# Optimization experiments

Hardware: AMD Instinct MI355X
Metric: run time of the kernel (lower is better)

## Reference

```python
import jax, jax.numpy as jnp
import numpy as np

B, NS, D, H, L, NQ, NK = 32, 4096, 256, 4, 6, 512, 1024
DH = D // H
SCALE = 1.0 / np.sqrt(DH)


def _ln(x, scale, bias, eps=1e-5):
    m = jnp.mean(x, axis=-1, keepdims=True)
    v = jnp.mean((x - m) ** 2, axis=-1, keepdims=True)
    return (x - m) * jax.lax.rsqrt(v + eps) * scale + bias


def setup_inputs() -> dict:
    key = jax.random.key(0)
    ks = jax.random.split(key, 12)
    d = {
        'update_tensor': jax.random.normal(ks[0], (B, NS, D), jnp.float32) * 0.1,
        'emb_table': jax.random.normal(ks[1], (NS + 1, D), jnp.float32) * 0.1,
        'mask_logits': jax.random.uniform(ks[2], (L, NQ, NK), jnp.float32),
        'Wq': jax.random.normal(ks[3], (D, D), jnp.float32) * 0.05,
        'Wk': jax.random.normal(ks[4], (D, D), jnp.float32) * 0.05,
        'Wv': jax.random.normal(ks[5], (D, D), jnp.float32) * 0.05,
        'Wo': jax.random.normal(ks[6], (D, D), jnp.float32) * 0.05,
        'W1': jax.random.normal(ks[7], (D, D), jnp.float32) * 0.05,
        'b1': jnp.zeros((D,), jnp.float32),
        'W2': jax.random.normal(ks[8], (D, D), jnp.float32) * 0.05,
        'b2': jnp.zeros((D,), jnp.float32),
        'sys_scale': jnp.ones((D,), jnp.float32),
        'sys_bias': jnp.zeros((D,), jnp.float32),
        'eff_scale': jnp.ones((D,), jnp.float32),
        'eff_bias': jnp.zeros((D,), jnp.float32),
        'inner_scale': jnp.ones((D,), jnp.float32),
        'inner_bias': jnp.zeros((D,), jnp.float32),
        'outer_scale': jnp.ones((D,), jnp.float32),
        'outer_bias': jnp.zeros((D,), jnp.float32),
        'query_idx': jax.random.randint(ks[9], (L, NQ), 0, NS).astype(jnp.int32),
        'key_idx': jax.random.randint(ks[10], (L, NK), 0, NS).astype(jnp.int32),
    }
    return d


def _hitr(q, k, mask, Wq, Wk, Wv, Wo, W1, b1, W2, b2, in_s, in_b, out_s, out_b):
    # q: [B,NQ,D] (pre-normed), k: [B,NK,D], mask: [NQ,NK] bool
    Q = jnp.einsum('bqd,de->bqe', q, Wq).reshape(B, NQ, H, DH)
    K = jnp.einsum('bkd,de->bke', k, Wk).reshape(B, NK, H, DH)
    V = jnp.einsum('bkd,de->bke', k, Wv).reshape(B, NK, H, DH)
    scores = jnp.einsum('bqhd,bkhd->bhqk', Q, K) * SCALE
    scores = jnp.where(mask[None, None], scores, jnp.float32(-1e9))
    attn = jax.nn.softmax(scores, axis=-1)
    ctx = jnp.einsum('bhqk,bkhd->bqhd', attn, V).reshape(B, NQ, D)
    h = _ln(jnp.einsum('bqd,de->bqe', ctx, Wo), in_s, in_b)
    ffn = jnp.einsum('bqd,de->bqe', jax.nn.gelu(jnp.einsum('bqd,de->bqe', h, W1) + b1), W2) + b2
    return _ln(h + ffn, out_s, out_b)


def reference(update_tensor, emb_table, mask_logits, Wq, Wk, Wv, Wo, W1, b1, W2, b2,
              sys_scale, sys_bias, eff_scale, eff_bias, inner_scale, inner_bias,
              outer_scale, outer_bias, query_idx, key_idx):
    update_result = jnp.zeros_like(update_tensor)
    for l in range(L):  # static hierarchy levels
        qi, ki = query_idx[l], key_idx[l]
        mask = mask_logits[l] > 0.5
        q = _ln(emb_table[qi][None] + update_tensor[:, qi], sys_scale, sys_bias)
        k = _ln(emb_table[ki][None] + update_tensor[:, ki], sys_scale, sys_bias)
        res = _ln(_hitr(q, k, mask, Wq, Wk, Wv, Wo, W1, b1, W2, b2,
                        inner_scale, inner_bias, outer_scale, outer_bias),
                  eff_scale, eff_bias)
        update_tensor = update_tensor.at[:, qi].add(res)
        update_result = update_result.at[:, qi].add(res)
    return update_result
```

## Files before the change

kernel.cpp:

```cpp
#include <hip/hip_runtime.h>
#include <cstdint>
#include <cstddef>

#define B_ 32
#define NS_ 4096
#define D_ 256
#define H_ 4
#define L_ 6
#define NQ_ 512
#define NK_ 1024
#define DH_ 64
#define SCALE_ 0.125f

typedef unsigned short ushort_t;
typedef unsigned long long u64_t;
typedef __bf16 bf16x8 __attribute__((ext_vector_type(8)));
typedef float f32x4 __attribute__((ext_vector_type(4)));

__device__ __forceinline__ ushort_t f2bf(float f) {
  unsigned u = __float_as_uint(f);
  u += 0x7fffu + ((u >> 16) & 1u);
  return (ushort_t)(u >> 16);
}

__device__ __forceinline__ void gld16(const void* g, void* l) {
  __builtin_amdgcn_global_load_lds(
      (__attribute__((address_space(1))) void*)(uintptr_t)g,
      (__attribute__((address_space(3))) void*)(uintptr_t)l, 16, 0, 0);
}

__global__ __launch_bounds__(256) void prep_w(
    const float* __restrict__ w0, const float* __restrict__ w1,
    const float* __restrict__ w2, const float* __restrict__ w3,
    const float* __restrict__ w4, const float* __restrict__ w5,
    ushort_t* __restrict__ wt) {
  const int sel = blockIdx.x >> 8;
  const int n = blockIdx.x & 255;
  const int k = threadIdx.x;
  const float* W = sel == 0 ? w0 : sel == 1 ? w1 : sel == 2 ? w2
                 : sel == 3 ? w3 : sel == 4 ? w4 : w5;
  wt[sel * 65536 + n * 256 + k] = f2bf(W[k * 256 + n]);
}

__global__ __launch_bounds__(256) void prep_mask(
    const float* __restrict__ ml, u64_t* __restrict__ mb) {
  const long gid = (long)blockIdx.x * 256 + threadIdx.x;
  const bool m = ml[gid] > 0.5f;
  const u64_t bal = __ballot(m);
  if ((threadIdx.x & 63) == 0) mb[gid >> 6] = bal;
}

__global__ __launch_bounds__(256) void prep_mask2(
    const u64_t* __restrict__ mb, u64_t* __restrict__ pm) {
  const long gid = (long)blockIdx.x * 256 + threadIdx.x;
  const long rowbase = (gid >> 4) << 4;
  const int l16 = (int)(gid & 15);
  u64_t v = 0;
#pragma unroll
  for (int kt = 0; kt < 16; ++kt) {
    const u64_t wsrc = mb[rowbase + kt];
#pragma unroll
    for (int ni = 0; ni < 4; ++ni)
      v |= ((wsrc >> (ni * 16 + l16)) & 1ull) << (kt * 4 + ni);
  }
  pm[gid] = v;
}

__global__ __launch_bounds__(256) void gather_ln(
    const float* __restrict__ ut, const float* __restrict__ emb,
    const int* __restrict__ qidx, const int* __restrict__ kidx,
    const float* __restrict__ sc, const float* __restrict__ bi,
    ushort_t* __restrict__ qn, ushort_t* __restrict__ kn) {
  const int w = threadIdx.x >> 6, lane = threadIdx.x & 63;
  const int R = blockIdx.x * 4 + w;
  int bb, idx;
  ushort_t* dst;
  long drow;
  if (R < B_ * NQ_) {
    bb = R >> 9; idx = qidx[R & (NQ_ - 1)]; dst = qn; drow = R;
  } else {
    const int r2 = R - B_ * NQ_;
    bb = r2 >> 10; idx = kidx[r2 & (NK_ - 1)]; dst = kn; drow = r2;
  }
  const int c0 = lane * 4;
  const float4 e = *(const float4*)(emb + (long)idx * 256 + c0);
  const float4 u = *(const float4*)(ut + ((long)bb * NS_ + idx) * 256 + c0);
  float x0 = e.x + u.x, x1 = e.y + u.y, x2 = e.z + u.z, x3 = e.w + u.w;
  float s1 = x0 + x1 + x2 + x3;
  float s2 = x0 * x0 + x1 * x1 + x2 * x2 + x3 * x3;
#pragma unroll
  for (int off = 1; off < 64; off <<= 1) {
    s1 += __shfl_xor(s1, off);
    s2 += __shfl_xor(s2, off);
  }
  const float mean = s1 * (1.f / 256.f);
  const float inv = rsqrtf(s2 * (1.f / 256.f) - mean * mean + 1e-5f);
  const float4 scv = *(const float4*)(sc + c0);
  const float4 biv = *(const float4*)(bi + c0);
  ushort4 o;
  o.x = f2bf((x0 - mean) * inv * scv.x + biv.x);
  o.y = f2bf((x1 - mean) * inv * scv.y + biv.y);
  o.z = f2bf((x2 - mean) * inv * scv.z + biv.z);
  o.w = f2bf((x3 - mean) * inv * scv.w + biv.w);
  *(ushort4*)(dst + drow * 256 + c0) = o;
}

template <int EPI>
__device__ __forceinline__ void gemm_body(
    const ushort_t* __restrict__ A, const ushort_t* __restrict__ Bt,
    void* __restrict__ Cout, long m0, int n0, ushort_t* lAB) {
  ushort_t* lA = lAB;
  ushort_t* lB = lAB + 8192;
  const int tid = threadIdx.x;
  const int lane = tid & 63, w = tid >> 6;
  const int quad = lane >> 4, l16 = lane & 15;
  const int wm = w & 1, wn = w >> 1;

  f32x4 acc[4][4] = {};

  for (int kt = 0; kt < 4; ++kt) {
    const int k0 = kt * 64;
#pragma unroll
    for (int p = 0; p < 4; ++p) {
      const int ob = p * 4096 + tid * 16;
      const int row = ob >> 7;
      const int chunk = ((ob >> 4) & 7) ^ (row & 7);
      gld16(A + (m0 + row) * 256 + k0 + chunk * 8, (char*)lA + p * 4096 + w * 1024);
      gld16(Bt + (long)(n0 + row) * 256 + k0 + chunk * 8, (char*)lB + p * 4096 + w * 1024);
    }
    __syncthreads();
#pragma unroll
    for (int ki = 0; ki < 2; ++ki) {
      bf16x8 af[4], bfr[4];
#pragma unroll
      for (int i = 0; i < 4; ++i) {
        const int ra = wm * 64 + i * 16 + l16;
        const int ca = (ki * 4 + quad) ^ (ra & 7);
        af[i] = *(const bf16x8*)&lA[ra * 64 + ca * 8];
        const int rb = wn * 64 + i * 16 + l16;
        const int cb = (ki * 4 + quad) ^ (rb & 7);
        bfr[i] = *(const bf16x8*)&lB[rb * 64 + cb * 8];
      }
#pragma unroll
      for (int mi = 0; mi < 4; ++mi)
#pragma unroll
        for (int ni = 0; ni < 4; ++ni)
          acc[mi][ni] = __builtin_amdgcn_mfma_f32_16x16x32_bf16(af[mi], bfr[ni], acc[mi][ni], 0, 0, 0);
    }
    __syncthreads();
  }

  if (EPI == 4) {
    const long b = m0 >> 10;
    const int kvseg = (int)(m0 & 1023);
#pragma unroll
    for (int hg = 0; hg < 2; ++hg) {
      if (wn == hg) {
#pragma unroll
        for (int mi = 0; mi < 4; ++mi)
#pragma unroll
          for (int ni = 0; ni < 4; ++ni)
#pragma unroll
            for (int r = 0; r < 4; ++r) {
              const int dh = ni * 16 + l16;
              const int kvl = wm * 64 + mi * 16 + quad * 4 + r;
              lAB[dh * 128 + (((kvl >> 3) ^ (dh & 15)) << 3) + (kvl & 7)] =
                  f2bf(acc[mi][ni][r]);
            }
      }
      __syncthreads();
      {
        const int dh = tid >> 2;
        const int head = (n0 >> 6) + hg;
        ushort_t* dst = (ushort_t*)Cout +
            ((b * 4 + head) * 64 + dh) * 1024 + kvseg;
#pragma unroll
        for (int i = 0; i < 4; ++i) {
          const int c = (tid & 3) * 4 + i;
          const int cs = c ^ (dh & 15);
          *(uint4*)(dst + c * 8) = *(const uint4*)&lAB[dh * 128 + cs * 8];
        }
      }
      __syncthreads();
    }
    return;
  }

#pragma unroll
  for (int mi = 0; mi < 4; ++mi) {
#pragma unroll
    for (int ni = 0; ni < 4; ++ni) {
#pragma unroll
      for (int r = 0; r < 4; ++r) {
        const long row = m0 + wm * 64 + mi * 16 + quad * 4 + r;
        const int col = n0 + wn * 64 + ni * 16 + l16;
        float v = acc[mi][ni][r];
        if (EPI == 5) v *= SCALE_;
        ((ushort_t*)Cout)[row * 256 + col] = f2bf(v);
      }
    }
  }
}

__global__ __launch_bounds__(256) void gemm_qkv(
    const ushort_t* __restrict__ qn, const ushort_t* __restrict__ kn,
    const ushort_t* __restrict__ wt,
    ushort_t* __restrict__ Qb, ushort_t* __restrict__ Kb, ushort_t* __restrict__ Vt) {
  __shared__ ushort_t lAB[16384];
  int idx = blockIdx.x;
  if (idx < 256) {
    gemm_body<5>(qn, wt, Qb, (long)(idx & 127) * 128, (idx >> 7) * 128, lAB);
  } else if (idx < 768) {
    idx -= 256;
    gemm_body<0>(kn, wt + 65536, Kb, (long)(idx & 255) * 128, (idx >> 8) * 128, lAB);
  } else {
    idx -= 768;
    gemm_body<4>(kn, wt + 131072, Vt, (long)(idx & 255) * 128, (idx >> 8) * 128, lAB);
  }
}

template <int MODE>
__global__ __launch_bounds__(256) void gemm_band(
    const ushort_t* __restrict__ A, const ushort_t* __restrict__ Bt,
    const float* __restrict__ bias,
    const float* __restrict__ ln1s, const float* __restrict__ ln1b,
    const float* __restrict__ ln2s, const float* __restrict__ ln2b,
    const float* __restrict__ hfres, const int* __restrict__ qidx,
    float* __restrict__ outF, ushort_t* __restrict__ outB,
    float* __restrict__ ut, float* __restrict__ out) {
  __shared__ ushort_t lA[3][2048];
  __shared__ ushort_t lB[3][8192];
  __shared__ float sS1[64][4], sS2[64][4];
  const int tid = threadIdx.x;
  const int lane = tid & 63, w = tid >> 6;
  const int quad = lane >> 4, l16 = lane & 15;
  const long m0 = (long)blockIdx.x * 64;

  auto stage = [&](int kt, int bu) {
    const int k0 = kt * 32;
    {
      const int ob = tid * 16;
      const int row = ob >> 6;
      const int c = (ob >> 4) & 3;
      gld16(A + (m0 + row) * 256 + k0 + (c ^ ((row >> 1) & 3)) * 8,
            (char*)&lA[bu][0] + w * 1024);
    }
#pragma unroll
    for (int p = 0; p < 4; ++p) {
      const int ob = p * 4096 + tid * 16;
      const int row = ob >> 6;
      const int c = (ob >> 4) & 3;
      gld16(Bt + (long)row * 256 + k0 + (c ^ ((row >> 1) & 3)) * 8,
            (char*)&lB[bu][0] + p * 4096 + w * 1024);
    }
  };

  f32x4 acc[4][4] = {};
  stage(0, 0);
  stage(1, 1);
#pragma unroll
  for (int kt = 0; kt < 8; ++kt) {
    const int bu = kt % 3;
    if (kt < 6) stage(kt + 2, (kt + 2) % 3);
    if (kt < 6)       asm volatile("s_waitcnt vmcnt(10)" ::: "memory");
    else if (kt == 6) asm volatile("s_waitcnt vmcnt(5)" ::: "memory");
    else              asm volatile("s_waitcnt vmcnt(0)" ::: "memory");
    __builtin_amdgcn_s_barrier();
    __builtin_amdgcn_sched_barrier(0);
    bf16x8 af[4], bfr[4];
#pragma unroll
    for (int i = 0; i < 4; ++i) {
      const int ra = i * 16 + l16;
      af[i] = *(const bf16x8*)&lA[bu][ra * 32 + ((quad ^ ((ra >> 1) & 3)) * 8)];
      const int rb = w * 64 + i * 16 + l16;
      bfr[i] = *(const bf16x8*)&lB[bu][rb * 32 + ((quad ^ ((rb >> 1) & 3)) * 8)];
    }
#pragma unroll
    for (int mi = 0; mi < 4; ++mi)
#pragma unroll
      for (int ni = 0; ni < 4; ++ni)
        acc[mi][ni] = __builtin_amdgcn_mfma_f32_16x16x32_bf16(af[mi], bfr[ni], acc[mi][ni], 0, 0, 0);
    __builtin_amdgcn_sched_barrier(0);
    __builtin_amdgcn_s_barrier();
  }

  if (MODE == 2) {
    float bcol[4];
#pragma unroll
    for (int ni = 0; ni < 4; ++ni) bcol[ni] = bias[w * 64 + ni * 16 + l16];
#pragma unroll
    for (int mi = 0; mi < 4; ++mi)
#pragma unroll
      for (int r = 0; r < 4; ++r) {
        const long row = m0 + mi * 16 + quad * 4 + r;
#pragma unroll
        for (int ni = 0; ni < 4; ++ni) {
          float v = acc[mi][ni][r] + bcol[ni];
          const float u = 0.7978845608028654f * (v + 0.044715f * v * v * v);
          v = 0.5f * v * (1.0f + tanhf(u));
          outB[row * 256 + (w * 64 + ni * 16 + l16)] = f2bf(v);
        }
      }
    return;
  }

  if (MODE == 6) {
#pragma unroll
    for (int mi = 0; mi < 4; ++mi)
#pragma unroll
      for (int r = 0; r < 4; ++r) {
        float a1 = 0.f, a2 = 0.f;
#pragma unroll
        for (int ni = 0; ni < 4; ++ni) {
          const float v = acc[mi][ni][r];
          a1 += v; a2 += v * v;
        }
#pragma unroll
        for (int off = 1; off < 16; off <<= 1) {
          a1 += __shfl_xor(a1, off);
          a2 += __shfl_xor(a2, off);
        }
        if (l16 == 0) {
          sS1[mi * 16 + quad * 4 + r][w] = a1;
          sS2[mi * 16 + quad * 4 + r][w] = a2;
        }
      }
    __syncthreads();
    float l1sv[4], l1bv[4];
#pragma unroll
    for (int ni = 0; ni < 4; ++ni) {
      const int col = w * 64 + ni * 16 + l16;
      l1sv[ni] = ln1s[col]; l1bv[ni] = ln1b[col];
    }
#pragma unroll
    for (int mi = 0; mi < 4; ++mi)
#pragma unroll
      for (int r = 0; r < 4; ++r) {
        const int rowi = mi * 16 + quad * 4 + r;
        const f32x4 v1 = *(const f32x4*)&sS1[rowi][0];
        const f32x4 v2 = *(const f32x4*)&sS2[rowi][0];
        const float s1 = v1[0] + v1[1] + v1[2] + v1[3];
        const float s2 = v2[0] + v2[1] + v2[2] + v2[3];
        const float mean = s1 * (1.f / 256.f);
        const float inv = rsqrtf(s2 * (1.f / 256.f) - mean * mean + 1e-5f);
        const long row = m0 + rowi;
#pragma unroll
        for (int ni = 0; ni < 4; ++ni) {
          const int col = w * 64 + ni * 16 + l16;
          const float y = (acc[mi][ni][r] - mean) * inv * l1sv[ni] + l1bv[ni];
          outF[row * 256 + col] = y;
          outB[row * 256 + col] = f2bf(y);
        }
      }
    return;
  }

  {
    float bcol[4], l1sv[4], l1bv[4], l2sv[4], l2bv[4];
#pragma unroll
    for (int ni = 0; ni < 4; ++ni) {
      const int col = w * 64 + ni * 16 + l16;
      bcol[ni] = bias[col];
      l1sv[ni] = ln1s[col]; l1bv[ni] = ln1b[col];
      l2sv[ni] = ln2s[col]; l2bv[ni] = ln2b[col];
    }
#pragma unroll
    for (int mi = 0; mi < 4; ++mi)
#pragma unroll
      for (int r = 0; r < 4; ++r) {
        const long row = m0 + mi * 16 + quad * 4 + r;
        float a1 = 0.f, a2 = 0.f;
#pragma unroll
        for (int ni = 0; ni < 4; ++ni) {
          const int col = w * 64 + ni * 16 + l16;
          const float v = acc[mi][ni][r] + bcol[ni] + hfres[row * 256 + col];
          acc[mi][ni][r] = v;
          a1 += v; a2 += v * v;
        }
#pragma unroll
        for (int off = 1; off < 16; off <<= 1) {
          a1 += __shfl_xor(a1, off);
          a2 += __shfl_xor(a2, off);
        }
        if (l16 == 0) {
          sS1[mi * 16 + quad * 4 + r][w] = a1;
          sS2[mi * 16 + quad * 4 + r][w] = a2;
        }
      }
    __syncthreads();
    float py1[4][4], py2[4][4];
#pragma unroll
    for (int mi = 0; mi < 4; ++mi)
#pragma unroll
      for (int r = 0; r < 4; ++r) {
        const int rowi = mi * 16 + quad * 4 + r;
        const f32x4 v1 = *(const f32x4*)&sS1[rowi][0];
        const f32x4 v2 = *(const f32x4*)&sS2[rowi][0];
        const float s1 = v1[0] + v1[1] + v1[2] + v1[3];
        const float s2 = v2[0] + v2[1] + v2[2] + v2[3];
        const float mean = s1 * (1.f / 256.f);
        const float inv = rsqrtf(s2 * (1.f / 256.f) - mean * mean + 1e-5f);
        float a1 = 0.f, a2 = 0.f;
#pragma unroll
        for (int ni = 0; ni < 4; ++ni) {
          const float y = (acc[mi][ni][r] - mean) * inv * l1sv[ni] + l1bv[ni];
          acc[mi][ni][r] = y;
          a1 += y; a2 += y * y;
        }
        py1[mi][r] = a1; py2[mi][r] = a2;
      }
    __syncthreads();
#pragma unroll
    for (int mi = 0; mi < 4; ++mi)
#pragma unroll
      for (int r = 0; r < 4; ++r) {
        float a1 = py1[mi][r], a2 = py2[mi][r];
#pragma unroll
        for (int off = 1; off < 16; off <<= 1) {
          a1 += __shfl_xor(a1, off);
          a2 += __shfl_xor(a2, off);
        }
        if (l16 == 0) {
          sS1[mi * 16 + quad * 4 + r][w] = a1;
          sS2[mi * 16 + quad * 4 + r][w] = a2;
        }
      }
    __syncthreads();
#pragma unroll
    for (int mi = 0; mi < 4; ++mi)
#pragma unroll
      for (int r = 0; r < 4; ++r) {
        const int rowi = mi * 16 + quad * 4 + r;
        const f32x4 v1 = *(const f32x4*)&sS1[rowi][0];
        const f32x4 v2 = *(const f32x4*)&sS2[rowi][0];
        const float s1 = v1[0] + v1[1] + v1[2] + v1[3];
        const float s2 = v2[0] + v2[1] + v2[2] + v2[3];
        const float mean = s1 * (1.f / 256.f);
        const float inv = rsqrtf(s2 * (1.f / 256.f) - mean * mean + 1e-5f);
        const long row = m0 + rowi;
        const int idx = qidx[(int)(row & (NQ_ - 1))];
        const long base = ((row >> 9) * (long)NS_ + idx) * 256;
#pragma unroll
        for (int ni = 0; ni < 4; ++ni) {
          const int col = w * 64 + ni * 16 + l16;
          const float z = (acc[mi][ni][r] - mean) * inv * l2sv[ni] + l2bv[ni];
          atomicAdd(&ut[base + col], z);
          atomicAdd(&out[base + col], z);
        }
      }
  }
}

__global__ __launch_bounds__(256) void attn_kernel(
    const ushort_t* __restrict__ Qb, const ushort_t* __restrict__ Kb,
    const ushort_t* __restrict__ Vt, const u64_t* __restrict__ pm,
    ushort_t* __restrict__ ctx) {
  __shared__ ushort_t lK[2][4096];
  __shared__ ushort_t lVt[2][4096];
  __shared__ ushort_t lP[4096];
  const int tid = threadIdx.x;
  const int lane = tid & 63, w = tid >> 6;
  const int quad = lane >> 4, l16 = lane & 15;
  const int bid = blockIdx.x;
  const int qt = bid >> 7, pair = bid & 127;
  const int h = pair & 3, b = pair >> 2;
  const int q0 = qt * 64;
  const long qrow0 = (long)b * NQ_ + q0;
  const long krow0 = (long)b * NK_;
  const ushort_t* vbase = Vt + ((long)pair * 64) * 1024;

  const int rq = w * 16 + l16;
  bf16x8 qfr[2];
#pragma unroll
  for (int ki = 0; ki < 2; ++ki)
    qfr[ki] = *(const bf16x8*)&Qb[(qrow0 + rq) * 256 + h * 64 + (ki * 4 + quad) * 8];
  u64_t pmr[4];
#pragma unroll
  for (int r = 0; r < 4; ++r)
    pmr[r] = pm[(long)(q0 + w * 16 + quad * 4 + r) * 16 + l16];

  auto stageKV = [&](int kt, int bu) {
#pragma unroll
    for (int p = 0; p < 2; ++p) {
      const int ob = p * 4096 + tid * 16;
      const int row = ob >> 7;
      const int chunk = ((ob >> 4) & 7) ^ (row & 7);
      gld16(Kb + (krow0 + kt * 64 + row) * 256 + h * 64 + chunk * 8,
            (char*)&lK[bu][0] + p * 4096 + w * 1024);
      gld16(vbase + (long)row * 1024 + kt * 64 + chunk * 8,
            (char*)&lVt[bu][0] + p * 4096 + w * 1024);
    }
  };

  f32x4 o_acc[4] = {};
  f32x4 l_acc = {};
  bf16x8 ones;
#pragma unroll
  for (int i = 0; i < 8; ++i) ones[i] = (__bf16)1.0f;

  stageKV(0, 0);

  for (int kt = 0; kt < 16; ++kt) {
    const int bu = kt & 1;
    if (kt < 15) stageKV(kt + 1, bu ^ 1);
    if (kt < 15) asm volatile("s_waitcnt vmcnt(4)" ::: "memory");
    else         asm volatile("s_waitcnt vmcnt(0)" ::: "memory");
    __builtin_amdgcn_s_barrier();
    __builtin_amdgcn_sched_barrier(0);

    f32x4 s[4] = {};
    __builtin_amdgcn_s_setprio(1);
#pragma unroll
    for (int ki = 0; ki < 2; ++ki) {
#pragma unroll
      for (int ni = 0; ni < 4; ++ni) {
        const int rk = ni * 16 + l16;
        const int ck = (ki * 4 + quad) ^ (rk & 7);
        const bf16x8 kf = *(const bf16x8*)&lK[bu][rk * 64 + ck * 8];
        s[ni] = __builtin_amdgcn_mfma_f32_16x16x32_bf16(qfr[ki], kf, s[ni], 0, 0, 0);
      }
    }
    __builtin_amdgcn_s_setprio(0);

#pragma unroll
    for (int r = 0; r < 4; ++r) {
      const int rowp = w * 16 + quad * 4 + r;
#pragma unroll
      for (int ni = 0; ni < 4; ++ni) {
        const bool keep = (pmr[r] >> (kt * 4 + ni)) & 1ull;
        const float pv = keep ? __expf(s[ni][r]) : 0.f;
        const int col = ni * 16 + l16;
        lP[rowp * 64 + (((col >> 3) ^ (rowp & 7)) << 3) + (col & 7)] = f2bf(pv);
      }
    }

    __builtin_amdgcn_s_setprio(1);
#pragma unroll
    for (int ki = 0; ki < 2; ++ki) {
      const int rp = w * 16 + l16;
      const int cp = (ki * 4 + quad) ^ (rp & 7);
      const bf16x8 pf = *(const bf16x8*)&lP[rp * 64 + cp * 8];
      l_acc = __builtin_amdgcn_mfma_f32_16x16x32_bf16(pf, ones, l_acc, 0, 0, 0);
#pragma unroll
      for (int ni = 0; ni < 4; ++ni) {
        const int rv = ni * 16 + l16;
        const int cv = (ki * 4 + quad) ^ (rv & 7);
        const bf16x8 vf = *(const bf16x8*)&lVt[bu][rv * 64 + cv * 8];
        o_acc[ni] = __builtin_amdgcn_mfma_f32_16x16x32_bf16(pf, vf, o_acc[ni], 0, 0, 0);
      }
    }
    __builtin_amdgcn_s_setprio(0);
    __builtin_amdgcn_sched_barrier(0);
    __builtin_amdgcn_s_barrier();
  }

#pragma unroll
  for (int r = 0; r < 4; ++r) {
    const float inv = 1.0f / l_acc[r];
    const long rowg = qrow0 + w * 16 + quad * 4 + r;
#pragma unroll
    for (int ni = 0; ni < 4; ++ni) {
      const int col = h * 64 + ni * 16 + l16;
      ctx[rowg * 256 + col] = f2bf(o_acc[ni][r] * inv);
    }
  }
}

extern "C" void kernel_launch(void* const* d_in, const int* in_sizes, int n_in,
                              void* d_out, int out_size, void* d_ws, size_t ws_size,
                              hipStream_t stream) {
  float* ut = (float*)d_in[0];
  const float* emb = (const float*)d_in[1];
  const float* maskl = (const float*)d_in[2];
  const float* Wq = (const float*)d_in[3];
  const float* Wk = (const float*)d_in[4];
  const float* Wv = (const float*)d_in[5];
  const float* Wo = (const float*)d_in[6];
  const float* W1 = (const float*)d_in[7];
  const float* b1 = (const float*)d_in[8];
  const float* W2 = (const float*)d_in[9];
  const float* b2 = (const float*)d_in[10];
  const float* sys_s = (const float*)d_in[11];
  const float* sys_b = (const float*)d_in[12];
  const float* eff_s = (const float*)d_in[13];
  const float* eff_b = (const float*)d_in[14];
  const float* in_s = (const float*)d_in[15];
  const float* in_b = (const float*)d_in[16];
  const float* out_s = (const float*)d_in[17];
  const float* out_b = (const float*)d_in[18];
  const int* qidx = (const int*)d_in[19];
  const int* kidx = (const int*)d_in[20];
  float* out = (float*)d_out;

  char* p = (char*)d_ws;
  auto carve = [&](size_t bytes) {
    void* r = (void*)p;
    p += (bytes + 255) & ~(size_t)255;
    return r;
  };
  ushort_t* wt = (ushort_t*)carve((size_t)6 * 65536 * 2);
  u64_t* mb = (u64_t*)carve((size_t)L_ * NQ_ * (NK_ / 64) * 8);
  u64_t* pmw = (u64_t*)carve((size_t)L_ * NQ_ * 16 * 8);
  ushort_t* qn = (ushort_t*)carve((size_t)16384 * 256 * 2);
  ushort_t* kn = (ushort_t*)carve((size_t)32768 * 256 * 2);
  ushort_t* Qb = (ushort_t*)carve((size_t)16384 * 256 * 2);
  ushort_t* Kb = (ushort_t*)carve((size_t)32768 * 256 * 2);
  ushort_t* Vt = (ushort_t*)carve((size_t)32768 * 256 * 2);

  ushort_t* ctx = qn;
  ushort_t* g = Qb;
  ushort_t* hb = Kb;
  float* hf = (float*)Vt;

  hipMemsetAsync(d_out, 0, (size_t)out_size, stream);
  prep_w<<<1536, 256, 0, stream>>>(Wq, Wk, Wv, Wo, W1, W2, wt);
  prep_mask<<<(L_ * NQ_ * NK_) / 256, 256, 0, stream>>>(maskl, mb);
  prep_mask2<<<(L_ * NQ_ * 16) / 256, 256, 0, stream>>>(mb, pmw);

  for (int l = 0; l < L_; ++l) {
    gather_ln<<<B_ * (NQ_ + NK_) / 4, 256, 0, stream>>>(
        ut, emb, qidx + l * NQ_, kidx + l * NK_, sys_s, sys_b, qn, kn);
    gemm_qkv<<<1280, 256, 0, stream>>>(qn, kn, wt, Qb, Kb, Vt);
    attn_kernel<<<1024, 256, 0, stream>>>(
        Qb, Kb, Vt, pmw + (size_t)l * NQ_ * 16, ctx);
    gemm_band<6><<<256, 256, 0, stream>>>(
        ctx, wt + 3 * 65536, nullptr, in_s, in_b, nullptr, nullptr,
        nullptr, nullptr, hf, hb, nullptr, nullptr);
    gemm_band<2><<<256, 256, 0, stream>>>(
        hb, wt + 4 * 65536, b1, nullptr, nullptr, nullptr, nullptr,
        nullptr, nullptr, nullptr, g, nullptr, nullptr);
    gemm_band<7><<<256, 256, 0, stream>>>(
        g, wt + 5 * 65536, b2, out_s, out_b, eff_s, eff_b,
        hf, qidx + l * NQ_, nullptr, nullptr, ut, out);
  }
}
```

Before: 1.231 ms.

## Double-buffer GEMM LDS tiles with async prefetch of next K-slice

Restructures the shared GEMM body from four K=64 steps with load-then-compute into eight K=32 steps, using two LDS buffers. The next slice is issued with direct global-to-LDS loads before computing on the current one, with partial vmcnt waits so memory latency overlaps the MFMA work. The swizzle is changed to fit the narrower 32-wide rows. This doubles the number of barriers per tile and uses smaller per-step MFMA batches.

Result: slower. 1.626 ms (+32.1%).

```diff
diff --git a/kernel.cpp b/kernel.cpp
--- a/kernel.cpp
+++ b/kernel.cpp
@@ -108,46 +108,52 @@
 template <int EPI>
 __device__ __forceinline__ void gemm_body(
     const ushort_t* __restrict__ A, const ushort_t* __restrict__ Bt,
-    void* __restrict__ Cout, long m0, int n0, ushort_t* lAB) {
-  ushort_t* lA = lAB;
-  ushort_t* lB = lAB + 8192;
+    void* __restrict__ Cout, long m0, int n0, ushort_t* lds) {
+  ushort_t* lA[2] = { lds, lds + 4096 };
+  ushort_t* lB[2] = { lds + 8192, lds + 12288 };
   const int tid = threadIdx.x;
   const int lane = tid & 63, w = tid >> 6;
   const int quad = lane >> 4, l16 = lane & 15;
   const int wm = w & 1, wn = w >> 1;
 
+  auto stage = [&](int kt, int bu) {
+    const int k0 = kt * 32;
+#pragma unroll
+    for (int p = 0; p < 2; ++p) {
+      const int ob = p * 4096 + tid * 16;
+      const int row = ob >> 6;
+      const int c = (ob >> 4) & 3;
+      const int chunk = c ^ ((row >> 1) & 3);
+      gld16(A + (m0 + row) * 256 + k0 + chunk * 8, (char*)lA[bu] + p * 4096 + w * 1024);
+      gld16(Bt + (long)(n0 + row) * 256 + k0 + chunk * 8, (char*)lB[bu] + p * 4096 + w * 1024);
+    }
+  };
+
   f32x4 acc[4][4] = {};
-
-  for (int kt = 0; kt < 4; ++kt) {
-    const int k0 = kt * 64;
-#pragma unroll
-    for (int p = 0; p < 4; ++p) {
-      const int ob = p * 4096 + tid * 16;
-      const int row = ob >> 7;
-      const int chunk = ((ob >> 4) & 7) ^ (row & 7);
-      gld16(A + (m0 + row) * 256 + k0 + chunk * 8, (char*)lA + p * 4096 + w * 1024);
-      gld16(Bt + (long)(n0 + row) * 256 + k0 + chunk * 8, (char*)lB + p * 4096 + w * 1024);
-    }
-    __syncthreads();
-#pragma unroll
-    for (int ki = 0; ki < 2; ++ki) {
-      bf16x8 af[4], bfr[4];
-#pragma unroll
-      for (int i = 0; i < 4; ++i) {
-        const int ra = wm * 64 + i * 16 + l16;
-        const int ca = (ki * 4 + quad) ^ (ra & 7);
-        af[i] = *(const bf16x8*)&lA[ra * 64 + ca * 8];
-        const int rb = wn * 64 + i * 16 + l16;
-        const int cb = (ki * 4 + quad) ^ (rb & 7);
-        bfr[i] = *(const bf16x8*)&lB[rb * 64 + cb * 8];
-      }
-#pragma unroll
-      for (int mi = 0; mi < 4; ++mi)
-#pragma unroll
-        for (int ni = 0; ni < 4; ++ni)
-          acc[mi][ni] = __builtin_amdgcn_mfma_f32_16x16x32_bf16(af[mi], bfr[ni], acc[mi][ni], 0, 0, 0);
-    }
-    __syncthreads();
+  stage(0, 0);
+#pragma unroll
+  for (int kt = 0; kt < 8; ++kt) {
+    const int bu = kt & 1;
+    if (kt < 7) stage(kt + 1, bu ^ 1);
+    if (kt < 7) asm volatile("s_waitcnt vmcnt(4)" ::: "memory");
+    else        asm volatile("s_waitcnt vmcnt(0)" ::: "memory");
+    __builtin_amdgcn_s_barrier();
+    __builtin_amdgcn_sched_barrier(0);
+    bf16x8 af[4], bfr[4];
+#pragma unroll
+    for (int i = 0; i < 4; ++i) {
+      const int ra = wm * 64 + i * 16 + l16;
+      af[i] = *(const bf16x8*)&lA[bu][ra * 32 + ((quad ^ ((ra >> 1) & 3)) * 8)];
+      const int rb = wn * 64 + i * 16 + l16;
+      bfr[i] = *(const bf16x8*)&lB[bu][rb * 32 + ((quad ^ ((rb >> 1) & 3)) * 8)];
+    }
+#pragma unroll
+    for (int mi = 0; mi < 4; ++mi)
+#pragma unroll
+      for (int ni = 0; ni < 4; ++ni)
+        acc[mi][ni] = __builtin_amdgcn_mfma_f32_16x16x32_bf16(af[mi], bfr[ni], acc[mi][ni], 0, 0, 0);
+    __builtin_amdgcn_sched_barrier(0);
+    __builtin_amdgcn_s_barrier();
   }
 
   if (EPI == 4) {
@@ -164,7 +170,7 @@
             for (int r = 0; r < 4; ++r) {
               const int dh = ni * 16 + l16;
               const int kvl = wm * 64 + mi * 16 + quad * 4 + r;
-              lAB[dh * 128 + (((kvl >> 3) ^ (dh & 15)) << 3) + (kvl & 7)] =
+              lds[dh * 128 + (((kvl >> 3) ^ (dh & 15)) << 3) + (kvl & 7)] =
                   f2bf(acc[mi][ni][r]);
             }
       }
@@ -178,7 +184,7 @@
         for (int i = 0; i < 4; ++i) {
           const int c = (tid & 3) * 4 + i;
           const int cs = c ^ (dh & 15);
-          *(uint4*)(dst + c * 8) = *(const uint4*)&lAB[dh * 128 + cs * 8];
+          *(uint4*)(dst + c * 8) = *(const uint4*)&lds[dh * 128 + cs * 8];
         }
       }
       __syncthreads();
```
